# Performance work log

Hardware: AMD Instinct MI355X
Metric: run time of the kernel (lower is better)

## Reference

```python
import jax, jax.numpy as jnp
import numpy as np

H = 16          # num_heads
KVH = 4         # num_kv_heads
HD = 128        # head_dim = dim // num_heads
BASE = 10000.0  # rope_base
EPS = 1.1920928955078125e-07  # torch F.rms_norm default eps = finfo(fp32).eps


def rotate_half(x):
    h = x.shape[-1] // 2
    return jnp.concatenate([-x[..., h:], x[..., :h]], axis=-1)


def rms_norm(x):
    return x * jax.lax.rsqrt(jnp.mean(x * x, axis=-1, keepdims=True) + EPS)


def setup_inputs() -> dict:
    key = jax.random.key(0)
    ks = jax.random.split(key, 5)
    D = H * HD
    KVD = KVH * HD
    s = 0.02
    x = jax.random.normal(ks[0], (4, 2048, D), jnp.float32)
    Wq = jax.random.normal(ks[1], (D, D), jnp.float32) * s
    Wk = jax.random.normal(ks[2], (KVD, D), jnp.float32) * s
    Wv = jax.random.normal(ks[3], (KVD, D), jnp.float32) * s
    Wproj = jax.random.normal(ks[4], (D, D), jnp.float32) * s
    q_gain = jnp.full((H,), 1.0, jnp.float32)
    return {"x": x, "Wq": Wq, "Wk": Wk, "Wv": Wv, "Wproj": Wproj, "q_gain": q_gain}


def reference(x, Wq, Wk, Wv, Wproj, q_gain):
    B, T, D = x.shape
    # QKV projections (bias-free), reshape to [B, heads, T, head_dim]
    q = (x @ Wq.T).reshape(B, T, H, HD).transpose(0, 2, 1, 3)
    k = (x @ Wk.T).reshape(B, T, KVH, HD).transpose(0, 2, 1, 3)
    v = (x @ Wv.T).reshape(B, T, KVH, HD).transpose(0, 2, 1, 3)
    # QK RMSNorm (no learned weight)
    q = rms_norm(q)
    k = rms_norm(k)
    # Rotary embedding tables [T, HD]
    t = jnp.arange(T, dtype=jnp.float32)
    inv_freq = 1.0 / (BASE ** (jnp.arange(0, HD, 2, dtype=jnp.float32) / HD))
    freqs = jnp.outer(t, inv_freq)
    emb = jnp.concatenate([freqs, freqs], axis=-1)
    cos, sin = jnp.cos(emb), jnp.sin(emb)
    # RoPE + per-head gain on q
    q = (q * cos + rotate_half(q) * sin) * q_gain[None, :, None, None]
    k = k * cos + rotate_half(k) * sin
    # GQA: repeat_interleave kv heads to match q heads
    groups = H // KVH
    k = jnp.repeat(k, groups, axis=1)
    v = jnp.repeat(v, groups, axis=1)
    # Causal scaled dot-product attention
    scores = jnp.einsum('bhqd,bhkd->bhqk', q, k) / np.float32(np.sqrt(HD))
    mask = jnp.tril(jnp.ones((T, T), dtype=bool))
    scores = jnp.where(mask, scores, -jnp.inf)
    attn = jax.nn.softmax(scores, axis=-1)
    y = jnp.einsum('bhqk,bhkd->bhqd', attn, v)
    y = y.transpose(0, 2, 1, 3).reshape(B, T, D)
    return y @ Wproj.T
```

## Files before the change

kernel.cpp:

```cpp
#include <hip/hip_runtime.h>
#include <math.h>


typedef float f32x4 __attribute__((ext_vector_type(4)));
typedef __bf16 bf16x8 __attribute__((ext_vector_type(8)));
typedef __bf16 bf16x4 __attribute__((ext_vector_type(4)));

__device__ __forceinline__ void load_lds16(const __bf16* g, __bf16* l) {
    __builtin_amdgcn_global_load_lds(
        (const __attribute__((address_space(1))) void*)g,
        (__attribute__((address_space(3))) void*)l, 16, 0, 0);
}

__global__ __launch_bounds__(256) void cvt_f32_bf16(
    const float* __restrict__ src, __bf16* __restrict__ dst, int n)
{
    int i = (blockIdx.x * 256 + threadIdx.x) * 4;
    if (i < n) {
        float4 v = *(const float4*)(src + i);
        bf16x4 o = {(__bf16)v.x, (__bf16)v.y, (__bf16)v.z, (__bf16)v.w};
        *(bf16x4*)(dst + i) = o;
    }
}

template <typename OutT>
__global__ __launch_bounds__(256) void gemm_bt(
    const __bf16* __restrict__ A, const __bf16* __restrict__ W,
    OutT* __restrict__ C, int M, int N, int K)
{
    const int bn = blockIdx.x, bm = blockIdx.y;
    const int tid = threadIdx.x;
    const int wave = tid >> 6, lane = tid & 63;
    const int quad = lane >> 4, l16 = lane & 15;

    __shared__ __bf16 As[128 * 32];
    __shared__ __bf16 Ws[128 * 32];

    const int wm = (wave & 1) * 64;
    const int wn = (wave >> 1) * 64;

    f32x4 acc[4][4] = {};

    const int srow = wave * 16 + (lane >> 2);
    const int scol = (lane & 3) * 8;

    const __bf16* Ag = A + (size_t)(bm * 128) * K + scol;
    const __bf16* Wg = W + (size_t)(bn * 128) * K + scol;

    for (int k0 = 0; k0 < K; k0 += 32) {
        __syncthreads();
#pragma unroll
        for (int r = 0; r < 2; ++r) {
            load_lds16(Ag + (size_t)(srow + r * 64) * K + k0, As + (r * 4 + wave) * 512);
            load_lds16(Wg + (size_t)(srow + r * 64) * K + k0, Ws + (r * 4 + wave) * 512);
        }
        __syncthreads();

        bf16x8 af[4], wf[4];
#pragma unroll
        for (int i = 0; i < 4; ++i) {
            af[i] = *(const bf16x8*)(As + (wm + i * 16 + l16) * 32 + quad * 8);
            wf[i] = *(const bf16x8*)(Ws + (wn + i * 16 + l16) * 32 + quad * 8);
        }
#pragma unroll
        for (int mi = 0; mi < 4; ++mi)
#pragma unroll
            for (int ni = 0; ni < 4; ++ni)
                acc[mi][ni] = __builtin_amdgcn_mfma_f32_16x16x32_bf16(
                    af[mi], wf[ni], acc[mi][ni], 0, 0, 0);
    }

#pragma unroll
    for (int mi = 0; mi < 4; ++mi) {
#pragma unroll
        for (int r = 0; r < 4; ++r) {
            int row = bm * 128 + wm + mi * 16 + quad * 4 + r;
            OutT* Cp = C + (size_t)row * N + bn * 128 + wn + l16;
#pragma unroll
            for (int ni = 0; ni < 4; ++ni)
                Cp[ni * 16] = (OutT)acc[mi][ni][r];
        }
    }
}

__global__ __launch_bounds__(256) void qk_norm_rope(
    __bf16* __restrict__ q, __bf16* __restrict__ kv,
    const float* __restrict__ q_gain)
{
    const int row = blockIdx.x * 4 + (threadIdx.x >> 6);
    const int lane = threadIdx.x & 63;
    const int BTH = 4 * 2048 * 16;

    __bf16* base;
    int t;
    float gain;
    if (row < BTH) {
        int bt = row >> 4, h = row & 15;
        base = q + (size_t)bt * 2048 + h * 128;
        t = bt & 2047;
        gain = q_gain[h];
    } else {
        int r2 = row - BTH;
        int bt = r2 >> 2, kvh = r2 & 3;
        base = kv + (size_t)bt * 1024 + kvh * 128;
        t = bt & 2047;
        gain = 1.0f;
    }

    float x0 = (float)base[lane];
    float x1 = (float)base[lane + 64];

    float ss = x0 * x0 + x1 * x1;
#pragma unroll
    for (int off = 32; off; off >>= 1) ss += __shfl_xor(ss, off);
    float inv = rsqrtf(ss * (1.0f / 128.0f) + 1.1920928955078125e-07f);
    x0 *= inv; x1 *= inv;

    float freq = exp2f(-(float)lane * 0.20762050593046013f);
    float ang = (float)t * freq;
    float s, c;
    sincosf(ang, &s, &c);
    float o0 = x0 * c - x1 * s;
    float o1 = x1 * c + x0 * s;
    base[lane]      = (__bf16)(o0 * gain);
    base[lane + 64] = (__bf16)(o1 * gain);
}

__global__ __launch_bounds__(256) void transpose_v(
    const __bf16* __restrict__ kv, __bf16* __restrict__ vtout)
{
    __shared__ __bf16 tile[64][65];
    const int b = blockIdx.z;
    const int t0 = blockIdx.x * 64, c0 = blockIdx.y * 64;
    const __bf16* vb = kv + (size_t)b * 2048 * 1024 + 512;
    __bf16* vtb = vtout + (size_t)b * 512 * 2048;
    const int j = threadIdx.x & 63;
    const int r0 = threadIdx.x >> 6;
#pragma unroll
    for (int i = 0; i < 16; ++i) {
        int r = r0 + i * 4;
        tile[r][j] = vb[(size_t)(t0 + r) * 1024 + c0 + j];
    }
    __syncthreads();
#pragma unroll
    for (int i = 0; i < 16; ++i) {
        int r = r0 + i * 4;
        vtb[(size_t)(c0 + r) * 2048 + t0 + j] = tile[j][r];
    }
}

__global__ __launch_bounds__(256, 2) void attn(
    const __bf16* __restrict__ q, const __bf16* __restrict__ kv,
    const __bf16* __restrict__ vt, __bf16* __restrict__ y,
    const float* __restrict__ q_gain)
{
    const int qt = 15 - blockIdx.y;
    const int bh = blockIdx.x;
    const int b = bh >> 4, h = bh & 15, kvh = h >> 2;
    const int tid = threadIdx.x;
    const int wave = tid >> 6, lane = tid & 63;
    const int quad = lane >> 4, l16 = lane & 15;

    __shared__ __bf16 Ks[2][64 * 128];
    __shared__ __bf16 Vts[2][128 * 64];
    __shared__ __bf16 Ps[4 * 16 * 64];

    const int qt0 = qt * 128;
    const int wq = wave * 16;

    bf16x8 qf[2][4];
#pragma unroll
    for (int p = 0; p < 2; ++p) {
        const size_t qrow =
            ((size_t)b * 2048 + qt0 + p * 64 + wq + l16) * 2048 + h * 128;
#pragma unroll
        for (int t = 0; t < 4; ++t)
            qf[p][t] = *(const bf16x8*)(q + qrow + t * 32 + quad * 8);
    }

    f32x4 oacc[2][8] = {};
    float lsum[2][4] = {};

    const float sm_scale = 0.12754635f;
    const float mfix = 11.5f * fabsf(q_gain[h]);

    const size_t kbase = (size_t)b * 2048 * 1024 + kvh * 128;
    const size_t vtbase = (size_t)(b * 4 + kvh) * 128 * 2048;

    const int rowK = lane >> 4, pcK = lane & 15;
    const int rowV = lane >> 3, pcV = lane & 7;

    const int nj = 2 * qt + 2;

    {
#pragma unroll
        for (int r = 0; r < 4; ++r) {
            int rrK = (r * 4 + wave) * 4 + rowK;
            int cK = pcK ^ (rrK & 15);
            load_lds16(kv + kbase + (size_t)rrK * 1024 + cK * 8,
                       &Ks[0][(r * 4 + wave) * 512]);
            int rrV = (r * 4 + wave) * 8 + rowV;
            int cV = pcV ^ (rrV & 7);
            load_lds16(vt + vtbase + (size_t)rrV * 2048 + cV * 8,
                       &Vts[0][(r * 4 + wave) * 512]);
        }
    }

    for (int jt = 0; jt < nj; ++jt) {
        const int cur = jt & 1;

        asm volatile("" ::: "memory");
        __builtin_amdgcn_s_barrier();
        asm volatile("" ::: "memory");

        if (jt + 1 < nj) {
            const int j0n = (jt + 1) * 64;
#pragma unroll
            for (int r = 0; r < 4; ++r) {
                int rrK = (r * 4 + wave) * 4 + rowK;
                int cK = pcK ^ (rrK & 15);
                load_lds16(kv + kbase + (size_t)(j0n + rrK) * 1024 + cK * 8,
                           &Ks[cur ^ 1][(r * 4 + wave) * 512]);
                int rrV = (r * 4 + wave) * 8 + rowV;
                int cV = pcV ^ (rrV & 7);
                load_lds16(vt + vtbase + (size_t)rrV * 2048 + j0n + cV * 8,
                           &Vts[cur ^ 1][(r * 4 + wave) * 512]);
            }
            asm volatile("s_waitcnt vmcnt(8)" ::: "memory");
        } else {
            asm volatile("s_waitcnt vmcnt(0)" ::: "memory");
        }

        asm volatile("" ::: "memory");
        __builtin_amdgcn_s_barrier();
        asm volatile("" ::: "memory");

        const __bf16* Kc = Ks[cur];
        const __bf16* Vc = Vts[cur];

#pragma unroll
        for (int p = 0; p < 2; ++p) {
            const int dlim = 2 * qt + p;
            if (jt > dlim) continue;

            f32x4 sacc[4] = {};
#pragma unroll
            for (int nt = 0; nt < 4; ++nt)
#pragma unroll
                for (int t = 0; t < 4; ++t) {
                    bf16x8 kf = *(const bf16x8*)(
                        Kc + (nt * 16 + l16) * 128 + ((t * 4 + quad) ^ l16) * 8);
                    sacc[nt] = __builtin_amdgcn_mfma_f32_16x16x32_bf16(
                        qf[p][t], kf, sacc[nt], 0, 0, 0);
                }

            if (jt == dlim) {
#pragma unroll
                for (int nt = 0; nt < 4; ++nt) {
                    int kg = nt * 16 + l16;
#pragma unroll
                    for (int r = 0; r < 4; ++r)
                        if (kg > wq + quad * 4 + r) sacc[nt][r] = -3.0e38f;
                }
            }

            float pv4[4][4];
#pragma unroll
            for (int nt = 0; nt < 4; ++nt)
#pragma unroll
                for (int r = 0; r < 4; ++r) {
                    float pv = exp2f((sacc[nt][r] - mfix) * sm_scale);
                    pv4[nt][r] = pv;
                    lsum[p][r] += pv;
                }

            __bf16* Pw = Ps + wave * 1024;
#pragma unroll
            for (int nt = 0; nt < 4; ++nt)
#pragma unroll
                for (int r = 0; r < 4; ++r) {
                    int row = quad * 4 + r;
                    int pc = (nt * 2 + (l16 >> 3)) ^ (row & 7);
                    Pw[row * 64 + pc * 8 + (l16 & 7)] = (__bf16)pv4[nt][r];
                }

#pragma unroll
            for (int kt = 0; kt < 2; ++kt) {
                bf16x8 pf = *(const bf16x8*)(
                    Pw + l16 * 64 + ((kt * 4 + quad) ^ (l16 & 7)) * 8);
#pragma unroll
                for (int vn = 0; vn < 8; ++vn) {
                    bf16x8 vf = *(const bf16x8*)(
                        Vc + (vn * 16 + l16) * 64 + ((kt * 4 + quad) ^ (l16 & 7)) * 8);
                    oacc[p][vn] = __builtin_amdgcn_mfma_f32_16x16x32_bf16(
                        pf, vf, oacc[p][vn], 0, 0, 0);
                }
            }
        }
    }

#pragma unroll
    for (int p = 0; p < 2; ++p) {
#pragma unroll
        for (int r = 0; r < 4; ++r)
#pragma unroll
            for (int off = 8; off; off >>= 1)
                lsum[p][r] += __shfl_xor(lsum[p][r], off);

        const size_t ybase =
            ((size_t)b * 2048 + qt0 + p * 64 + wq) * 2048 + h * 128;
#pragma unroll
        for (int r = 0; r < 4; ++r) {
            float inv = 1.0f / lsum[p][r];
            __bf16* yp = y + ybase + (size_t)(quad * 4 + r) * 2048 + l16;
#pragma unroll
            for (int vn = 0; vn < 8; ++vn)
                yp[vn * 16] = (__bf16)(oacc[p][vn][r] * inv);
        }
    }
}

extern "C" void kernel_launch(void* const* d_in, const int* in_sizes, int n_in,
                              void* d_out, int out_size, void* d_ws, size_t ws_size,
                              hipStream_t stream) {
    const float* x     = (const float*)d_in[0];
    const float* Wq    = (const float*)d_in[1];
    const float* Wk    = (const float*)d_in[2];
    const float* Wv    = (const float*)d_in[3];
    const float* Wproj = (const float*)d_in[4];
    const float* qgain = (const float*)d_in[5];
    float* outp = (float*)d_out;

    __bf16* xb  = (__bf16*)d_ws;
    __bf16* Wqb = xb  + 16777216;
    __bf16* Wkb = Wqb + 4194304;
    __bf16* Wvb = Wkb + 1048576;
    __bf16* Wpb = Wvb + 1048576;
    __bf16* q   = Wpb + 4194304;
    __bf16* kvb = q   + 16777216;
    __bf16* vt  = kvb + 8388608;
    __bf16* y   = q;

    dim3 blk(256);
    cvt_f32_bf16<<<dim3(16777216 / 1024), blk, 0, stream>>>(x, xb, 16777216);
    cvt_f32_bf16<<<dim3(4194304 / 1024), blk, 0, stream>>>(Wq, Wqb, 4194304);
    cvt_f32_bf16<<<dim3(1048576 / 1024), blk, 0, stream>>>(Wk, Wkb, 1048576);
    cvt_f32_bf16<<<dim3(1048576 / 1024), blk, 0, stream>>>(Wv, Wvb, 1048576);
    cvt_f32_bf16<<<dim3(4194304 / 1024), blk, 0, stream>>>(Wproj, Wpb, 4194304);

    gemm_bt<__bf16><<<dim3(16, 64), blk, 0, stream>>>(xb, Wqb, q, 8192, 2048, 2048);
    gemm_bt<__bf16><<<dim3(8, 64), blk, 0, stream>>>(xb, Wkb, kvb, 8192, 1024, 2048);
    qk_norm_rope<<<dim3((4 * 2048 * (16 + 4)) / 4), blk, 0, stream>>>(q, kvb, qgain);
    transpose_v<<<dim3(32, 8, 4), blk, 0, stream>>>(kvb, vt);
    attn<<<dim3(64, 16), blk, 0, stream>>>(q, kvb, vt, y, qgain);
    gemm_bt<float><<<dim3(16, 64), blk, 0, stream>>>(y, Wpb, outp, 8192, 2048, 2048);
}
```

Measured before the change: 556.1 us.

## Replace GEMM with 256-row double-buffered swizzled-LDS 512-thread kernel

```diff
diff --git a/kernel.cpp b/kernel.cpp
--- a/kernel.cpp
+++ b/kernel.cpp
@@ -23,61 +23,123 @@
     }
 }
 
-template <typename OutT>
-__global__ __launch_bounds__(256) void gemm_bt(
+template <int NI, typename OutT>
+__global__ __launch_bounds__(512, 2) void gemm256(
     const __bf16* __restrict__ A, const __bf16* __restrict__ W,
     OutT* __restrict__ C, int M, int N, int K)
 {
+    constexpr int BN = 64 * NI;
     const int bn = blockIdx.x, bm = blockIdx.y;
     const int tid = threadIdx.x;
-    const int wave = tid >> 6, lane = tid & 63;
+    const int lane = tid & 63;
+    const int wave = tid >> 6;
     const int quad = lane >> 4, l16 = lane & 15;
-
-    __shared__ __bf16 As[128 * 32];
-    __shared__ __bf16 Ws[128 * 32];
-
-    const int wm = (wave & 1) * 64;
-    const int wn = (wave >> 1) * 64;
-
-    f32x4 acc[4][4] = {};
-
-    const int srow = wave * 16 + (lane >> 2);
-    const int scol = (lane & 3) * 8;
-
-    const __bf16* Ag = A + (size_t)(bm * 128) * K + scol;
-    const __bf16* Wg = W + (size_t)(bn * 128) * K + scol;
-
-    for (int k0 = 0; k0 < K; k0 += 32) {
-        __syncthreads();
-#pragma unroll
-        for (int r = 0; r < 2; ++r) {
-            load_lds16(Ag + (size_t)(srow + r * 64) * K + k0, As + (r * 4 + wave) * 512);
-            load_lds16(Wg + (size_t)(srow + r * 64) * K + k0, Ws + (r * 4 + wave) * 512);
-        }
-        __syncthreads();
-
-        bf16x8 af[4], wf[4];
-#pragma unroll
-        for (int i = 0; i < 4; ++i) {
-            af[i] = *(const bf16x8*)(As + (wm + i * 16 + l16) * 32 + quad * 8);
-            wf[i] = *(const bf16x8*)(Ws + (wn + i * 16 + l16) * 32 + quad * 8);
-        }
-#pragma unroll
-        for (int mi = 0; mi < 4; ++mi)
-#pragma unroll
-            for (int ni = 0; ni < 4; ++ni)
-                acc[mi][ni] = __builtin_amdgcn_mfma_f32_16x16x32_bf16(
-                    af[mi], wf[ni], acc[mi][ni], 0, 0, 0);
-    }
-
-#pragma unroll
-    for (int mi = 0; mi < 4; ++mi) {
+    const int wm2 = wave >> 2;
+    const int wn4 = wave & 3;
+
+    __shared__ __bf16 As[2][256 * 64];
+    __shared__ __bf16 Bs[2][BN * 64];
+
+    f32x4 acc[8][NI] = {};
+
+    const int sr = tid >> 3;
+    const int sc = tid & 7;
+    const int scs = sc ^ (sr & 7);
+
+    const __bf16* Ag = A + (size_t)(bm * 256 + sr) * K + scs * 8;
+    const __bf16* Wg = W + (size_t)(bn * BN + sr) * K + scs * 8;
+    __bf16* Asd = &As[0][0] + sr * 64 + sc * 8;
+    __bf16* Bsd = &Bs[0][0] + sr * 64 + sc * 8;
+
+    auto stage = [&](int t, int h) {
+        const int k0 = t * 64;
+#pragma unroll
+        for (int ra = 0; ra < 4; ++ra)
+            load_lds16(Ag + (size_t)(ra * 64) * K + k0,
+                       Asd + h * 16384 + ra * 4096);
+#pragma unroll
+        for (int rb = 0; rb < NI; ++rb)
+            load_lds16(Wg + (size_t)(rb * 64) * K + k0,
+                       Bsd + h * (BN * 64) + rb * 4096);
+    };
+    auto wait_prev = [&]() {
+        if constexpr (NI == 4) asm volatile("s_waitcnt vmcnt(8)" ::: "memory");
+        else                   asm volatile("s_waitcnt vmcnt(6)" ::: "memory");
+    };
+
+    const int NT = K / 64;
+
+    stage(0, 0);
+    stage(1, 1);
+    wait_prev();
+    asm volatile("" ::: "memory");
+    __builtin_amdgcn_s_barrier();
+    asm volatile("" ::: "memory");
+
+    for (int t = 0; t < NT; ++t) {
+        const int h = t & 1;
+        const __bf16* Ab = &As[h][0];
+        const __bf16* Bb = &Bs[h][0];
+
+        bf16x8 bfr[NI][2];
+#pragma unroll
+        for (int ph = 0; ph < 4; ++ph) {
+            bf16x8 af[2][2];
+#pragma unroll
+            for (int j = 0; j < 2; ++j)
+#pragma unroll
+                for (int ks = 0; ks < 2; ++ks)
+                    af[j][ks] = *(const bf16x8*)(
+                        Ab + (wm2 * 128 + (ph * 2 + j) * 16 + l16) * 64 +
+                        (((ks * 4 + quad) ^ (l16 & 7)) * 8));
+            if (ph == 0) {
+#pragma unroll
+                for (int ni = 0; ni < NI; ++ni)
+#pragma unroll
+                    for (int ks = 0; ks < 2; ++ks)
+                        bfr[ni][ks] = *(const bf16x8*)(
+                            Bb + (wn4 * 16 * NI + ni * 16 + l16) * 64 +
+                            (((ks * 4 + quad) ^ (l16 & 7)) * 8));
+            }
+            asm volatile("" ::: "memory");
+            __builtin_amdgcn_s_barrier();
+            asm volatile("" ::: "memory");
+            __builtin_amdgcn_s_setprio(1);
+#pragma unroll
+            for (int j = 0; j < 2; ++j)
+#pragma unroll
+                for (int ni = 0; ni < NI; ++ni)
+#pragma unroll
+                    for (int ks = 0; ks < 2; ++ks)
+                        acc[ph * 2 + j][ni] = __builtin_amdgcn_mfma_f32_16x16x32_bf16(
+                            af[j][ks], bfr[ni][ks], acc[ph * 2 + j][ni], 0, 0, 0);
+            __builtin_amdgcn_s_setprio(0);
+            asm volatile("" ::: "memory");
+            __builtin_amdgcn_s_barrier();
+            asm volatile("" ::: "memory");
+        }
+
+        if (t + 2 < NT) {
+            stage(t + 2, h);
+            wait_prev();
+        } else if (t + 1 < NT) {
+            asm volatile("s_waitcnt vmcnt(0)" ::: "memory");
+        } else {
+            break;
+        }
+        asm volatile("" ::: "memory");
+        __builtin_amdgcn_s_barrier();
+        asm volatile("" ::: "memory");
+    }
+
+#pragma unroll
+    for (int mi = 0; mi < 8; ++mi) {
 #pragma unroll
         for (int r = 0; r < 4; ++r) {
-            int row = bm * 128 + wm + mi * 16 + quad * 4 + r;
-            OutT* Cp = C + (size_t)row * N + bn * 128 + wn + l16;
-#pragma unroll
-            for (int ni = 0; ni < 4; ++ni)
+            int row = bm * 256 + wm2 * 128 + mi * 16 + quad * 4 + r;
+            OutT* Cp = C + (size_t)row * N + bn * BN + wn4 * 16 * NI + l16;
+#pragma unroll
+            for (int ni = 0; ni < NI; ++ni)
                 Cp[ni * 16] = (OutT)acc[mi][ni][r];
         }
     }
@@ -348,10 +410,10 @@
     cvt_f32_bf16<<<dim3(1048576 / 1024), blk, 0, stream>>>(Wv, Wvb, 1048576);
     cvt_f32_bf16<<<dim3(4194304 / 1024), blk, 0, stream>>>(Wproj, Wpb, 4194304);
 
-    gemm_bt<__bf16><<<dim3(16, 64), blk, 0, stream>>>(xb, Wqb, q, 8192, 2048, 2048);
-    gemm_bt<__bf16><<<dim3(8, 64), blk, 0, stream>>>(xb, Wkb, kvb, 8192, 1024, 2048);
+    gemm256<4, __bf16><<<dim3(8, 32), dim3(512), 0, stream>>>(xb, Wqb, q, 8192, 2048, 2048);
+    gemm256<2, __bf16><<<dim3(8, 32), dim3(512), 0, stream>>>(xb, Wkb, kvb, 8192, 1024, 2048);
     qk_norm_rope<<<dim3((4 * 2048 * (16 + 4)) / 4), blk, 0, stream>>>(q, kvb, qgain);
     transpose_v<<<dim3(32, 8, 4), blk, 0, stream>>>(kvb, vt);
     attn<<<dim3(64, 16), blk, 0, stream>>>(q, kvb, vt, y, qgain);
-    gemm_bt<float><<<dim3(16, 64), blk, 0, stream>>>(y, Wpb, outp, 8192, 2048, 2048);
-}
+    gemm256<4, float><<<dim3(8, 32), dim3(512), 0, stream>>>(y, Wpb, outp, 8192, 2048, 2048);
+}
```

Measured after the change: 527.6 us. -5.1%, faster.
